# Kernel optimization log

Measured on AMD Instinct MI355X. Metric: run time of the kernel, lower is better.

The kernel has to match this reference:

```python
import jax, jax.numpy as jnp
import numpy as np

VOCAB = 32000   # vocab size
EDIM = 1024     # embedding dim
HDIM = 1024     # encoder hidden dim (fhid dim)
NACTS = 2       # ACTS = {'push': 0, 'pop': 1}
NCLASSES = 3
L = 256         # len_total
B = 128         # bsz
PAD = 0         # padding_idx
PUSH, POP = 0, 1


def setup_inputs() -> dict:
    key = jax.random.key(0)
    ks = jax.random.split(key, 10)

    def mk_seq(kt, kl):
        tok = jax.random.randint(kt, (L, B), 1, VOCAB)          # non-pad tokens
        lens = jax.random.randint(kl, (B,), L // 2, L - 1)      # ragged lengths
        t = jnp.arange(L)[:, None]
        # first lens+1 positions non-pad (so lens = L - n_pad - 1 as in the module)
        return jnp.where(t < lens[None, :] + 1, tok, PAD)

    seq1 = mk_seq(ks[0], ks[1])
    seq2 = mk_seq(ks[2], ks[3])

    def w(k, shp):
        return (jax.random.normal(k, shp, jnp.float32) * 0.02)

    return {
        "seq1": seq1, "seq2": seq2,
        "emb": w(ks[4], (VOCAB, EDIM)),
        "W_top": w(ks[5], (EDIM, HDIM)), "b_top": jnp.zeros((HDIM,), jnp.float32),
        "W_act": w(ks[6], (EDIM, NACTS)), "b_act": jnp.zeros((NACTS,), jnp.float32),
        "W1": w(ks[7], (4 * HDIM, HDIM)), "b1": jnp.zeros((HDIM,), jnp.float32),
        "W2": w(ks[8], (HDIM, NCLASSES)), "b2": jnp.zeros((NCLASSES,), jnp.float32),
    }


def _encode(seq, emb, W_top, b_top, W_act, b_act):
    # stub stack-encoder: time dim 2L-1 (one shift + one reduce step per token)
    seq_ext = jnp.concatenate([seq, seq[:-1]], axis=0)          # [2L-1, B]
    x = emb[seq_ext]                                            # [2L-1, B, E]
    top = jnp.tanh(jnp.einsum('tbe,eh->tbh', x, W_top) + b_top) # [2L-1, B, H]
    act = jax.nn.softmax(jnp.einsum('tbe,ea->tba', x, W_act) + b_act, axis=-1)
    return top, act


def _ragged_stats(act, Ts, bsz):
    # masked equivalents of the per-sample python loops over acts[:T, b, :]
    Tmax = act.shape[0]
    mask = (jnp.arange(Tmax)[:, None] < Ts[None, :]).astype(act.dtype)  # [2L-1, B]
    Tf = Ts.astype(act.dtype)
    push, pop = act[:, :, PUSH], act[:, :, POP]
    sum_push = (push * mask).sum(axis=0) / Tf                   # [B]
    sum_pop = ((pop * mask).sum(axis=0) + 1.0) / Tf             # [B]
    diff = jnp.sqrt((((push - pop) ** 2) * mask).sum(axis=0)) / Tf  # [B]
    dis = jnp.linalg.norm(sum_push - sum_pop) / bsz             # scalar
    return dis, diff.sum() / bsz


def reference(seq1, seq2, emb, W_top, b_top, W_act, b_act, W1, b1, W2, b2):
    bsz = seq1.shape[1]
    top1, act1 = _encode(seq1, emb, W_top, b_top, W_act, b_act)
    top2, act2 = _encode(seq2, emb, W_top, b_top, W_act, b_act)

    lens1 = seq1.shape[0] - (seq1 == PAD).sum(axis=0) - 1
    lens2 = seq2.shape[0] - (seq2 == PAD).sum(axis=0) - 1
    Ts1 = 2 * lens1 - 1
    Ts2 = 2 * lens2 - 1

    barange = jnp.arange(bsz)
    fhid1 = top1[Ts1 - 1, barange]                              # [B, H] ragged gather
    fhid2 = top2[Ts2 - 1, barange]

    u = jnp.concatenate([fhid1, fhid2, jnp.abs(fhid1 - fhid2), fhid1 * fhid2], axis=-1)
    res_clf = jax.nn.relu(u @ W1 + b1) @ W2 + b2                # [B, nclasses]

    dis1, diff1 = _ragged_stats(act1, Ts1, bsz)
    dis2, diff2 = _ragged_stats(act2, Ts2, bsz)
    return (res_clf, dis1, dis2, diff1, diff2)
```

## Files before the change

### kernel.cpp

```cpp
#include <hip/hip_runtime.h>
#include <math.h>

#define LL 256
#define BB 128
#define EDIM 1024
#define HDIM 1024
#define VOCAB 32000

#define NKSF 8
#define NKS  16

#define WS_EACT   0
#define WS_DELTA  32000
#define WS_DIFFB  32256
#define WS_FHID   33024
#define WS_BIG    295168

#define APAD 68

__device__ __forceinline__ void fma4(float4& a, float s, const float4& w) {
  a.x = fmaf(s, w.x, a.x); a.y = fmaf(s, w.y, a.y);
  a.z = fmaf(s, w.z, a.z); a.w = fmaf(s, w.w, a.w);
}

extern "C" __global__ __launch_bounds__(256)
void k_fh_eact(const float* __restrict__ emb, const float* __restrict__ Wtop,
               const float* __restrict__ Wact,
               const int* __restrict__ seq1, const int* __restrict__ seq2,
               float* __restrict__ fpart, float* __restrict__ Eact) {
  __shared__ float ash[128 * APAD];
  __shared__ int stok[128];
  int blk = blockIdx.x, tid = threadIdx.x;
  if (blk >= 256) {
    int lane = tid & 63, wave = tid >> 6;
    int v = (blk - 256) * 4 + wave;
    const float4* row = (const float4*)(emb + (size_t)v * EDIM);
    const float4* w4 = (const float4*)Wact;
    float a0 = 0.f;
#pragma unroll
    for (int it = 0; it < 4; ++it) {
      int i = lane + it * 64;
      float4 x = row[i];
      float4 wa = w4[2 * i];
      float4 wb = w4[2 * i + 1];
      a0 = fmaf(x.x, wa.x - wa.y, a0);
      a0 = fmaf(x.y, wa.z - wa.w, a0);
      a0 = fmaf(x.z, wb.x - wb.y, a0);
      a0 = fmaf(x.w, wb.z - wb.w, a0);
    }
#pragma unroll
    for (int off = 32; off; off >>= 1)
      a0 += __shfl_down(a0, off, 64);
    if (lane == 0) Eact[v] = a0;
    return;
  }
  int ks = blk >> 5, rb = (blk >> 4) & 1, cb = blk & 15;
  int cg = tid & 15, rgr = tid >> 4;
  int c0 = cb * 64 + cg * 4;
  int kbase = ks * 128;
  const int* seq = rb ? seq2 : seq1;
  {
    int c = tid >> 1, h = tid & 1;
    int z = 0;
    int base = h * 128;
    for (int r = 0; r < 128; ++r)
      z += (seq[(base + r) * BB + c] == 0) ? 1 : 0;
    z += __shfl_xor(z, 1, 64);
    if (h == 0) {
      int lens = 255 - z;
      int tt = 2 * lens - 2;
      int idx = (tt < LL) ? tt : tt - LL;
      stok[c] = seq[idx * BB + c];
    }
  }
  float4 acc[8];
#pragma unroll
  for (int r = 0; r < 8; ++r) acc[r] = make_float4(0.f, 0.f, 0.f, 0.f);
#pragma unroll
  for (int ch = 0; ch < 2; ++ch) {
    int kg = kbase + ch * 64;
    __syncthreads();
    for (int idx = tid; idx < 128 * 16; idx += 256) {
      int r = idx >> 4, q = idx & 15;
      *(float4*)&ash[r * APAD + q * 4] =
          ((const float4*)(emb + (size_t)stok[r] * EDIM + kg))[q];
    }
    __syncthreads();
    const float* Wp = Wtop + (size_t)kg * HDIM + c0;
    float4 w[4];
#pragma unroll
    for (int j = 0; j < 4; ++j) w[j] = *(const float4*)(Wp + (size_t)j * HDIM);
#pragma unroll
    for (int kk = 0; kk < 64; kk += 4) {
      float4 wn[4];
      if (kk + 4 < 64) {
#pragma unroll
        for (int j = 0; j < 4; ++j) wn[j] = *(const float4*)(Wp + (size_t)(kk + 4 + j) * HDIM);
      }
#pragma unroll
      for (int r = 0; r < 8; ++r) {
        float4 a = *(const float4*)&ash[(rgr * 8 + r) * APAD + kk];
        fma4(acc[r], a.x, w[0]); fma4(acc[r], a.y, w[1]);
        fma4(acc[r], a.z, w[2]); fma4(acc[r], a.w, w[3]);
      }
#pragma unroll
      for (int j = 0; j < 4; ++j) w[j] = wn[j];
    }
  }
  float* dst = fpart + ((size_t)ks * 256 + rb * 128 + rgr * 8) * HDIM + c0;
#pragma unroll
  for (int r = 0; r < 8; ++r)
    *(float4*)(dst + (size_t)r * HDIM) = acc[r];
}

extern "C" __global__ __launch_bounds__(256)
void k_ftanh_stats(const float* __restrict__ fpart, const float* __restrict__ btop,
                   const int* __restrict__ seq1, const int* __restrict__ seq2,
                   const float* __restrict__ Eact, const float* __restrict__ b_act,
                   float* __restrict__ fhid, float* __restrict__ delta,
                   float* __restrict__ diffb) {
  int blk = blockIdx.x, tid = threadIdx.x;
  if (blk < 256) {
    int g = blk * 256 + tid;
    float4 s = ((const float4*)fpart)[g];
#pragma unroll
    for (int k = 1; k < NKSF; ++k) {
      float4 p = ((const float4*)fpart)[(size_t)k * 65536 + g];
      s.x += p.x; s.y += p.y; s.z += p.z; s.w += p.w;
    }
    float4 b = ((const float4*)btop)[g & 255];
    ((float4*)fhid)[g] = make_float4(tanhf(s.x + b.x), tanhf(s.y + b.y),
                                     tanhf(s.z + b.z), tanhf(s.w + b.w));
    return;
  }
  int sb = blk - 256;
  int s = sb >> 7, b = sb & 127;
  const int* seq = s ? seq2 : seq1;
  __shared__ int col[LL];
  __shared__ int zred[256];
  __shared__ float redf[256];
  int v = seq[tid * BB + b];
  col[tid] = v;
  zred[tid] = (v == 0) ? 1 : 0;
  __syncthreads();
  for (int off = 128; off; off >>= 1) {
    if (tid < off) zred[tid] += zred[tid + off];
    __syncthreads();
  }
  int lens = LL - zred[0] - 1;
  int Ts = 2 * lens - 1;
  float ba = b_act[0] - b_act[1];
  float sp = 0.f, sq = 0.f;
  for (int t = tid; t < Ts; t += 256) {
    int tok = (t < LL) ? col[t] : col[t - LL];
    float d = Eact[tok] + ba;
    float p0 = 1.0f / (1.0f + expf(-d));
    float dd = 2.f * p0 - 1.f;
    sp += dd;
    sq = fmaf(dd, dd, sq);
  }
  redf[tid] = sp; __syncthreads();
  for (int off = 128; off; off >>= 1) { if (tid < off) redf[tid] += redf[tid + off]; __syncthreads(); }
  float tsp = redf[0]; __syncthreads();
  redf[tid] = sq; __syncthreads();
  for (int off = 128; off; off >>= 1) { if (tid < off) redf[tid] += redf[tid + off]; __syncthreads(); }
  if (tid == 0) {
    float Tf = (float)Ts;
    delta[sb] = (tsp - 1.0f) / Tf;
    diffb[sb] = sqrtf(redf[0]) / Tf;
  }
}

extern "C" __global__ __launch_bounds__(256)
void k_part(const float* __restrict__ fhid, const float* __restrict__ W1,
            float* __restrict__ part) {
  __shared__ float ush[64 * APAD];
  int blk = blockIdx.x, tid = threadIdx.x;
  int g = blk >> 1, rh = blk & 1;
  int ksb = g >> 4, cb = g & 15;
  int cg = tid & 15, rgr = tid >> 4;
  int c0 = cb * 64 + cg * 4;
  int m0 = rh * 64;
  int seg = ksb >> 2;
  const float4* f4 = (const float4*)fhid;
  float4 acc[4];
#pragma unroll
  for (int r = 0; r < 4; ++r) acc[r] = make_float4(0.f, 0.f, 0.f, 0.f);
  for (int kch = 0; kch < 4; ++kch) {
    int kg = ksb * 256 + kch * 64;
    int fb4 = (kg & 1023) >> 2;
    __syncthreads();
#pragma unroll
    for (int j = 0; j < 4; ++j) {
      int idx = tid + j * 256;
      int r = idx >> 4, q = idx & 15;
      int row = m0 + r;
      float4 uv;
      if (seg == 0) uv = f4[row * 256 + fb4 + q];
      else if (seg == 1) uv = f4[(128 + row) * 256 + fb4 + q];
      else {
        float4 f1v = f4[row * 256 + fb4 + q];
        float4 f2v = f4[(128 + row) * 256 + fb4 + q];
        if (seg == 2)
          uv = make_float4(fabsf(f1v.x - f2v.x), fabsf(f1v.y - f2v.y),
                           fabsf(f1v.z - f2v.z), fabsf(f1v.w - f2v.w));
        else
          uv = make_float4(f1v.x * f2v.x, f1v.y * f2v.y,
                           f1v.z * f2v.z, f1v.w * f2v.w);
      }
      *(float4*)&ush[r * APAD + q * 4] = uv;
    }
    __syncthreads();
    const float* Wp = W1 + (size_t)kg * HDIM + c0;
    float4 w[4];
#pragma unroll
    for (int j = 0; j < 4; ++j) w[j] = *(const float4*)(Wp + (size_t)j * HDIM);
#pragma unroll
    for (int kk = 0; kk < 64; kk += 4) {
      float4 wn[4];
      if (kk + 4 < 64) {
#pragma unroll
        for (int j = 0; j < 4; ++j)
          wn[j] = *(const float4*)(Wp + (size_t)(kk + 4 + j) * HDIM);
      }
#pragma unroll
      for (int r = 0; r < 4; ++r) {
        float4 a = *(const float4*)&ush[(rgr + 16 * r) * APAD + kk];
        fma4(acc[r], a.x, w[0]); fma4(acc[r], a.y, w[1]);
        fma4(acc[r], a.z, w[2]); fma4(acc[r], a.w, w[3]);
      }
#pragma unroll
      for (int j = 0; j < 4; ++j) w[j] = wn[j];
    }
  }
  float* dst = part + ((size_t)ksb * 128 + m0 + rgr) * HDIM + c0;
#pragma unroll
  for (int r = 0; r < 4; ++r)
    *(float4*)(dst + (size_t)r * 16 * HDIM) = acc[r];
}

extern "C" __global__ __launch_bounds__(256)
void k_clf_final(const float* __restrict__ part, const float* __restrict__ b1,
                 const float* __restrict__ W2, const float* __restrict__ b2,
                 const float* __restrict__ delta, const float* __restrict__ diffb,
                 float* __restrict__ out) {
  int blk = blockIdx.x, tid = threadIdx.x;
  __shared__ float red[768];
  if (blk == 128) {
    for (int s = 0; s < 2; ++s) {
      float v = 0.f, w = 0.f;
      if (tid < BB) { float d = delta[s * BB + tid]; v = d * d; w = diffb[s * BB + tid]; }
      red[tid] = v; __syncthreads();
      for (int off = 128; off; off >>= 1) { if (tid < off) red[tid] += red[tid + off]; __syncthreads(); }
      if (tid == 0) out[384 + s] = sqrtf(red[0]) / (float)BB;
      __syncthreads();
      red[tid] = w; __syncthreads();
      for (int off = 128; off; off >>= 1) { if (tid < off) red[tid] += red[tid + off]; __syncthreads(); }
      if (tid == 0) out[386 + s] = red[0] / (float)BB;
      __syncthreads();
    }
    return;
  }
  int b = blk;
  float4 p = ((const float4*)b1)[tid];
  const float4* p4 = (const float4*)part;
#pragma unroll
  for (int ks = 0; ks < NKS; ++ks) {
    float4 q = p4[((size_t)ks * 128 + b) * 256 + tid];
    p.x += q.x; p.y += q.y; p.z += q.z; p.w += q.w;
  }
  p.x = fmaxf(p.x, 0.f); p.y = fmaxf(p.y, 0.f);
  p.z = fmaxf(p.z, 0.f); p.w = fmaxf(p.w, 0.f);
  int k0 = tid * 4;
  float a0 = 0.f, a1 = 0.f, a2 = 0.f;
  a0 = fmaf(p.x, W2[(k0 + 0) * 3 + 0], a0); a1 = fmaf(p.x, W2[(k0 + 0) * 3 + 1], a1); a2 = fmaf(p.x, W2[(k0 + 0) * 3 + 2], a2);
  a0 = fmaf(p.y, W2[(k0 + 1) * 3 + 0], a0); a1 = fmaf(p.y, W2[(k0 + 1) * 3 + 1], a1); a2 = fmaf(p.y, W2[(k0 + 1) * 3 + 2], a2);
  a0 = fmaf(p.z, W2[(k0 + 2) * 3 + 0], a0); a1 = fmaf(p.z, W2[(k0 + 2) * 3 + 1], a1); a2 = fmaf(p.z, W2[(k0 + 2) * 3 + 2], a2);
  a0 = fmaf(p.w, W2[(k0 + 3) * 3 + 0], a0); a1 = fmaf(p.w, W2[(k0 + 3) * 3 + 1], a1); a2 = fmaf(p.w, W2[(k0 + 3) * 3 + 2], a2);
  red[tid] = a0; red[256 + tid] = a1; red[512 + tid] = a2;
  __syncthreads();
  for (int off = 128; off; off >>= 1) {
    if (tid < off) {
      red[tid] += red[tid + off];
      red[256 + tid] += red[256 + tid + off];
      red[512 + tid] += red[512 + tid + off];
    }
    __syncthreads();
  }
  if (tid == 0) {
    out[b * 3 + 0] = red[0]   + b2[0];
    out[b * 3 + 1] = red[256] + b2[1];
    out[b * 3 + 2] = red[512] + b2[2];
  }
}

extern "C" void kernel_launch(void* const* d_in, const int* in_sizes, int n_in,
                              void* d_out, int out_size, void* d_ws, size_t ws_size,
                              hipStream_t stream) {
  const int*   seq1  = (const int*)  d_in[0];
  const int*   seq2  = (const int*)  d_in[1];
  const float* emb   = (const float*)d_in[2];
  const float* W_top = (const float*)d_in[3];
  const float* b_top = (const float*)d_in[4];
  const float* W_act = (const float*)d_in[5];
  const float* b_act = (const float*)d_in[6];
  const float* W1    = (const float*)d_in[7];
  const float* b1    = (const float*)d_in[8];
  const float* W2    = (const float*)d_in[9];
  const float* b2    = (const float*)d_in[10];
  float* out = (float*)d_out;
  float* ws  = (float*)d_ws;

  float* Eact  = ws + WS_EACT;
  float* delta = ws + WS_DELTA;
  float* diffb = ws + WS_DIFFB;
  float* fhid  = ws + WS_FHID;
  float* bigb  = ws + WS_BIG;

  hipLaunchKernelGGL(k_fh_eact,     dim3(256 + 8000), dim3(256), 0, stream, emb, W_top, W_act, seq1, seq2, bigb, Eact);
  hipLaunchKernelGGL(k_ftanh_stats, dim3(512),        dim3(256), 0, stream, bigb, b_top, seq1, seq2, Eact, b_act, fhid, delta, diffb);
  hipLaunchKernelGGL(k_part,        dim3(512),        dim3(256), 0, stream, fhid, W1, bigb);
  hipLaunchKernelGGL(k_clf_final,   dim3(129),        dim3(256), 0, stream, bigb, b1, W2, b2, delta, diffb, out);
}
```

Baseline: 259.1 us.

## Retile W1 GEMM over all rows and fold ragged stats into it

The W1 partial-product kernel is retiled so each block covers all 128 batch rows over a 128-wide K slice, doubling the split-K count to 32. Each W1 tile is now read by one block instead of two row-halves. The per-sample ragged statistics move out of the tanh-reduction kernel and run as extra blocks of the GEMM launch, so they overlap with GEMM work. The first GEMM's shared-memory row mapping is also interleaved to ease LDS bank conflicts. The cost is twice as many partial sums for the final kernel to reduce, plus higher register use from 8 accumulators per thread.

```diff
diff --git a/kernel.cpp b/kernel.cpp
--- a/kernel.cpp
+++ b/kernel.cpp
@@ -8,7 +8,7 @@
 #define VOCAB 32000
 
 #define NKSF 8
-#define NKS  16
+#define NKS  32
 
 #define WS_EACT   0
 #define WS_DELTA  32000
@@ -99,7 +99,7 @@
       }
 #pragma unroll
       for (int r = 0; r < 8; ++r) {
-        float4 a = *(const float4*)&ash[(rgr * 8 + r) * APAD + kk];
+        float4 a = *(const float4*)&ash[(rgr + 16 * r) * APAD + kk];
         fma4(acc[r], a.x, w[0]); fma4(acc[r], a.y, w[1]);
         fma4(acc[r], a.z, w[2]); fma4(acc[r], a.w, w[3]);
       }
@@ -107,100 +107,99 @@
       for (int j = 0; j < 4; ++j) w[j] = wn[j];
     }
   }
-  float* dst = fpart + ((size_t)ks * 256 + rb * 128 + rgr * 8) * HDIM + c0;
+  float* dst = fpart + ((size_t)ks * 256 + rb * 128 + rgr) * HDIM + c0;
 #pragma unroll
   for (int r = 0; r < 8; ++r)
-    *(float4*)(dst + (size_t)r * HDIM) = acc[r];
+    *(float4*)(dst + (size_t)r * 16 * HDIM) = acc[r];
 }
 
 extern "C" __global__ __launch_bounds__(256)
-void k_ftanh_stats(const float* __restrict__ fpart, const float* __restrict__ btop,
-                   const int* __restrict__ seq1, const int* __restrict__ seq2,
-                   const float* __restrict__ Eact, const float* __restrict__ b_act,
-                   float* __restrict__ fhid, float* __restrict__ delta,
-                   float* __restrict__ diffb) {
+void k_ftanh(const float* __restrict__ fpart, const float* __restrict__ btop,
+             float* __restrict__ fhid) {
   int blk = blockIdx.x, tid = threadIdx.x;
-  if (blk < 256) {
-    int g = blk * 256 + tid;
-    float4 s = ((const float4*)fpart)[g];
-#pragma unroll
-    for (int k = 1; k < NKSF; ++k) {
-      float4 p = ((const float4*)fpart)[(size_t)k * 65536 + g];
-      s.x += p.x; s.y += p.y; s.z += p.z; s.w += p.w;
-    }
-    float4 b = ((const float4*)btop)[g & 255];
-    ((float4*)fhid)[g] = make_float4(tanhf(s.x + b.x), tanhf(s.y + b.y),
-                                     tanhf(s.z + b.z), tanhf(s.w + b.w));
+  int g = blk * 256 + tid;
+  float4 s = ((const float4*)fpart)[g];
+#pragma unroll
+  for (int k = 1; k < NKSF; ++k) {
+    float4 p = ((const float4*)fpart)[(size_t)k * 65536 + g];
+    s.x += p.x; s.y += p.y; s.z += p.z; s.w += p.w;
+  }
+  float4 b = ((const float4*)btop)[g & 255];
+  ((float4*)fhid)[g] = make_float4(tanhf(s.x + b.x), tanhf(s.y + b.y),
+                                   tanhf(s.z + b.z), tanhf(s.w + b.w));
+}
+
+extern "C" __global__ __launch_bounds__(256)
+void k_part_stats(const float* __restrict__ fhid, const float* __restrict__ W1,
+                  const int* __restrict__ seq1, const int* __restrict__ seq2,
+                  const float* __restrict__ Eact, const float* __restrict__ b_act,
+                  float* __restrict__ part, float* __restrict__ delta,
+                  float* __restrict__ diffb) {
+  __shared__ float ash[128 * APAD];
+  __shared__ int col[LL];
+  __shared__ float redf[256];
+  int blk = blockIdx.x, tid = threadIdx.x;
+  if (blk >= 512) {
+    int sb = blk - 512;
+    int s = sb >> 7, b = sb & 127;
+    const int* seq = s ? seq2 : seq1;
+    int* zred = (int*)ash;
+    int v = seq[tid * BB + b];
+    col[tid] = v;
+    zred[tid] = (v == 0) ? 1 : 0;
+    __syncthreads();
+    for (int off = 128; off; off >>= 1) {
+      if (tid < off) zred[tid] += zred[tid + off];
+      __syncthreads();
+    }
+    int lens = LL - zred[0] - 1;
+    int Ts = 2 * lens - 1;
+    float ba = b_act[0] - b_act[1];
+    float sp = 0.f, sq = 0.f;
+    for (int t = tid; t < Ts; t += 256) {
+      int tok = (t < LL) ? col[t] : col[t - LL];
+      float d = Eact[tok] + ba;
+      float p0 = 1.0f / (1.0f + expf(-d));
+      float dd = 2.f * p0 - 1.f;
+      sp += dd;
+      sq = fmaf(dd, dd, sq);
+    }
+    redf[tid] = sp; __syncthreads();
+    for (int off = 128; off; off >>= 1) { if (tid < off) redf[tid] += redf[tid + off]; __syncthreads(); }
+    float tsp = redf[0]; __syncthreads();
+    redf[tid] = sq; __syncthreads();
+    for (int off = 128; off; off >>= 1) { if (tid < off) redf[tid] += redf[tid + off]; __syncthreads(); }
+    if (tid == 0) {
+      float Tf = (float)Ts;
+      delta[sb] = (tsp - 1.0f) / Tf;
+      diffb[sb] = sqrtf(redf[0]) / Tf;
+    }
     return;
   }
-  int sb = blk - 256;
-  int s = sb >> 7, b = sb & 127;
-  const int* seq = s ? seq2 : seq1;
-  __shared__ int col[LL];
-  __shared__ int zred[256];
-  __shared__ float redf[256];
-  int v = seq[tid * BB + b];
-  col[tid] = v;
-  zred[tid] = (v == 0) ? 1 : 0;
-  __syncthreads();
-  for (int off = 128; off; off >>= 1) {
-    if (tid < off) zred[tid] += zred[tid + off];
-    __syncthreads();
-  }
-  int lens = LL - zred[0] - 1;
-  int Ts = 2 * lens - 1;
-  float ba = b_act[0] - b_act[1];
-  float sp = 0.f, sq = 0.f;
-  for (int t = tid; t < Ts; t += 256) {
-    int tok = (t < LL) ? col[t] : col[t - LL];
-    float d = Eact[tok] + ba;
-    float p0 = 1.0f / (1.0f + expf(-d));
-    float dd = 2.f * p0 - 1.f;
-    sp += dd;
-    sq = fmaf(dd, dd, sq);
-  }
-  redf[tid] = sp; __syncthreads();
-  for (int off = 128; off; off >>= 1) { if (tid < off) redf[tid] += redf[tid + off]; __syncthreads(); }
-  float tsp = redf[0]; __syncthreads();
-  redf[tid] = sq; __syncthreads();
-  for (int off = 128; off; off >>= 1) { if (tid < off) redf[tid] += redf[tid + off]; __syncthreads(); }
-  if (tid == 0) {
-    float Tf = (float)Ts;
-    delta[sb] = (tsp - 1.0f) / Tf;
-    diffb[sb] = sqrtf(redf[0]) / Tf;
-  }
-}
-
-extern "C" __global__ __launch_bounds__(256)
-void k_part(const float* __restrict__ fhid, const float* __restrict__ W1,
-            float* __restrict__ part) {
-  __shared__ float ush[64 * APAD];
-  int blk = blockIdx.x, tid = threadIdx.x;
-  int g = blk >> 1, rh = blk & 1;
-  int ksb = g >> 4, cb = g & 15;
+  int ksb = blk >> 4, cb = blk & 15;
   int cg = tid & 15, rgr = tid >> 4;
   int c0 = cb * 64 + cg * 4;
-  int m0 = rh * 64;
-  int seg = ksb >> 2;
+  int kbase = ksb * 128;
+  int seg = ksb >> 3;
   const float4* f4 = (const float4*)fhid;
-  float4 acc[4];
-#pragma unroll
-  for (int r = 0; r < 4; ++r) acc[r] = make_float4(0.f, 0.f, 0.f, 0.f);
-  for (int kch = 0; kch < 4; ++kch) {
-    int kg = ksb * 256 + kch * 64;
+  float4 acc[8];
+#pragma unroll
+  for (int r = 0; r < 8; ++r) acc[r] = make_float4(0.f, 0.f, 0.f, 0.f);
+#pragma unroll
+  for (int kch = 0; kch < 2; ++kch) {
+    int kg = kbase + kch * 64;
     int fb4 = (kg & 1023) >> 2;
     __syncthreads();
 #pragma unroll
-    for (int j = 0; j < 4; ++j) {
+    for (int j = 0; j < 8; ++j) {
       int idx = tid + j * 256;
       int r = idx >> 4, q = idx & 15;
-      int row = m0 + r;
       float4 uv;
-      if (seg == 0) uv = f4[row * 256 + fb4 + q];
-      else if (seg == 1) uv = f4[(128 + row) * 256 + fb4 + q];
+      if (seg == 0) uv = f4[r * 256 + fb4 + q];
+      else if (seg == 1) uv = f4[(128 + r) * 256 + fb4 + q];
       else {
-        float4 f1v = f4[row * 256 + fb4 + q];
-        float4 f2v = f4[(128 + row) * 256 + fb4 + q];
+        float4 f1v = f4[r * 256 + fb4 + q];
+        float4 f2v = f4[(128 + r) * 256 + fb4 + q];
         if (seg == 2)
           uv = make_float4(fabsf(f1v.x - f2v.x), fabsf(f1v.y - f2v.y),
                            fabsf(f1v.z - f2v.z), fabsf(f1v.w - f2v.w));
@@ -208,7 +207,7 @@
           uv = make_float4(f1v.x * f2v.x, f1v.y * f2v.y,
                            f1v.z * f2v.z, f1v.w * f2v.w);
       }
-      *(float4*)&ush[r * APAD + q * 4] = uv;
+      *(float4*)&ash[r * APAD + q * 4] = uv;
     }
     __syncthreads();
     const float* Wp = W1 + (size_t)kg * HDIM + c0;
@@ -224,8 +223,8 @@
           wn[j] = *(const float4*)(Wp + (size_t)(kk + 4 + j) * HDIM);
       }
 #pragma unroll
-      for (int r = 0; r < 4; ++r) {
-        float4 a = *(const float4*)&ush[(rgr + 16 * r) * APAD + kk];
+      for (int r = 0; r < 8; ++r) {
+        float4 a = *(const float4*)&ash[(rgr + 16 * r) * APAD + kk];
         fma4(acc[r], a.x, w[0]); fma4(acc[r], a.y, w[1]);
         fma4(acc[r], a.z, w[2]); fma4(acc[r], a.w, w[3]);
       }
@@ -233,9 +232,9 @@
       for (int j = 0; j < 4; ++j) w[j] = wn[j];
     }
   }
-  float* dst = part + ((size_t)ksb * 128 + m0 + rgr) * HDIM + c0;
-#pragma unroll
-  for (int r = 0; r < 4; ++r)
+  float* dst = part + ((size_t)ksb * 128 + rgr) * HDIM + c0;
+#pragma unroll
+  for (int r = 0; r < 8; ++r)
     *(float4*)(dst + (size_t)r * 16 * HDIM) = acc[r];
 }
 
@@ -317,8 +316,8 @@
   float* fhid  = ws + WS_FHID;
   float* bigb  = ws + WS_BIG;
 
-  hipLaunchKernelGGL(k_fh_eact,     dim3(256 + 8000), dim3(256), 0, stream, emb, W_top, W_act, seq1, seq2, bigb, Eact);
-  hipLaunchKernelGGL(k_ftanh_stats, dim3(512),        dim3(256), 0, stream, bigb, b_top, seq1, seq2, Eact, b_act, fhid, delta, diffb);
-  hipLaunchKernelGGL(k_part,        dim3(512),        dim3(256), 0, stream, fhid, W1, bigb);
-  hipLaunchKernelGGL(k_clf_final,   dim3(129),        dim3(256), 0, stream, bigb, b1, W2, b2, delta, diffb, out);
-}
+  hipLaunchKernelGGL(k_fh_eact,    dim3(256 + 8000), dim3(256), 0, stream, emb, W_top, W_act, seq1, seq2, bigb, Eact);
+  hipLaunchKernelGGL(k_ftanh,      dim3(256),        dim3(256), 0, stream, bigb, b_top, fhid);
+  hipLaunchKernelGGL(k_part_stats, dim3(768),        dim3(256), 0, stream, fhid, W1, seq1, seq2, Eact, b_act, bigb, delta, diffb);
+  hipLaunchKernelGGL(k_clf_final,  dim3(129),        dim3(256), 0, stream, bigb, b1, W2, b2, delta, diffb, out);
+}
```

Result: slower. 266.7 us (+2.9%).

## Spread vocab Eact projection across three kernels and fuse stats into final kernel

Applied to the files above, without the earlier changes.

The per-vocab W_act projection (Eact over all 32000 rows) is split into three chunks. Each chunk rides along as extra blocks in the first three kernels, so the bandwidth-heavy emb scan overlaps with the GEMM-like work instead of sitting mostly in the first kernel. The ragged activation stats move into the final classifier kernel and are reduced with atomics plus a last-block-done counter, which removes the separate delta/diffb workspace and the single-block reduction. The atomic float accumulation makes the reduction order nondeterministic, and it relies on the accumulator being zeroed early in the first kernel.

```diff
diff --git a/kernel.cpp b/kernel.cpp
--- a/kernel.cpp
+++ b/kernel.cpp
@@ -10,9 +10,12 @@
 #define NKSF 8
 #define NKS  16
 
+#define E1 3000
+#define E2 1000
+#define E3 4000
+
 #define WS_EACT   0
-#define WS_DELTA  32000
-#define WS_DIFFB  32256
+#define WS_ACC    32512
 #define WS_FHID   33024
 #define WS_BIG    295168
 
@@ -23,35 +26,44 @@
   a.z = fmaf(s, w.z, a.z); a.w = fmaf(s, w.w, a.w);
 }
 
+__device__ __forceinline__ void eact_row(const float* __restrict__ emb,
+                                         const float* __restrict__ Wact,
+                                         float* __restrict__ Eact,
+                                         int v, int lane) {
+  const float4* row = (const float4*)(emb + (size_t)v * EDIM);
+  const float4* w4 = (const float4*)Wact;
+  float a0 = 0.f;
+#pragma unroll
+  for (int it = 0; it < 4; ++it) {
+    int i = lane + it * 64;
+    float4 x = row[i];
+    float4 wa = w4[2 * i];
+    float4 wb = w4[2 * i + 1];
+    a0 = fmaf(x.x, wa.x - wa.y, a0);
+    a0 = fmaf(x.y, wa.z - wa.w, a0);
+    a0 = fmaf(x.z, wb.x - wb.y, a0);
+    a0 = fmaf(x.w, wb.z - wb.w, a0);
+  }
+#pragma unroll
+  for (int off = 32; off; off >>= 1)
+    a0 += __shfl_down(a0, off, 64);
+  if (lane == 0) Eact[v] = a0;
+}
+
 extern "C" __global__ __launch_bounds__(256)
-void k_fh_eact(const float* __restrict__ emb, const float* __restrict__ Wtop,
-               const float* __restrict__ Wact,
-               const int* __restrict__ seq1, const int* __restrict__ seq2,
-               float* __restrict__ fpart, float* __restrict__ Eact) {
+void k_fh_a(const float* __restrict__ emb, const float* __restrict__ Wtop,
+            const float* __restrict__ Wact,
+            const int* __restrict__ seq1, const int* __restrict__ seq2,
+            float* __restrict__ fpart, float* __restrict__ Eact,
+            float* __restrict__ accbuf) {
   __shared__ float ash[128 * APAD];
   __shared__ int stok[128];
   int blk = blockIdx.x, tid = threadIdx.x;
   if (blk >= 256) {
+    if (blk == 256 && tid < 8) accbuf[tid] = 0.f;
     int lane = tid & 63, wave = tid >> 6;
     int v = (blk - 256) * 4 + wave;
-    const float4* row = (const float4*)(emb + (size_t)v * EDIM);
-    const float4* w4 = (const float4*)Wact;
-    float a0 = 0.f;
-#pragma unroll
-    for (int it = 0; it < 4; ++it) {
-      int i = lane + it * 64;
-      float4 x = row[i];
-      float4 wa = w4[2 * i];
-      float4 wb = w4[2 * i + 1];
-      a0 = fmaf(x.x, wa.x - wa.y, a0);
-      a0 = fmaf(x.y, wa.z - wa.w, a0);
-      a0 = fmaf(x.z, wb.x - wb.y, a0);
-      a0 = fmaf(x.w, wb.z - wb.w, a0);
-    }
-#pragma unroll
-    for (int off = 32; off; off >>= 1)
-      a0 += __shfl_down(a0, off, 64);
-    if (lane == 0) Eact[v] = a0;
+    eact_row(emb, Wact, Eact, v, lane);
     return;
   }
   int ks = blk >> 5, rb = (blk >> 4) & 1, cb = blk & 15;
@@ -114,68 +126,42 @@
 }
 
 extern "C" __global__ __launch_bounds__(256)
-void k_ftanh_stats(const float* __restrict__ fpart, const float* __restrict__ btop,
-                   const int* __restrict__ seq1, const int* __restrict__ seq2,
-                   const float* __restrict__ Eact, const float* __restrict__ b_act,
-                   float* __restrict__ fhid, float* __restrict__ delta,
-                   float* __restrict__ diffb) {
+void k_tanh_b(const float* __restrict__ fpart, const float* __restrict__ btop,
+              float* __restrict__ fhid,
+              const float* __restrict__ emb, const float* __restrict__ Wact,
+              float* __restrict__ Eact) {
   int blk = blockIdx.x, tid = threadIdx.x;
-  if (blk < 256) {
-    int g = blk * 256 + tid;
-    float4 s = ((const float4*)fpart)[g];
-#pragma unroll
-    for (int k = 1; k < NKSF; ++k) {
-      float4 p = ((const float4*)fpart)[(size_t)k * 65536 + g];
-      s.x += p.x; s.y += p.y; s.z += p.z; s.w += p.w;
-    }
-    float4 b = ((const float4*)btop)[g & 255];
-    ((float4*)fhid)[g] = make_float4(tanhf(s.x + b.x), tanhf(s.y + b.y),
-                                     tanhf(s.z + b.z), tanhf(s.w + b.w));
+  if (blk >= 256) {
+    int lane = tid & 63, wave = tid >> 6;
+    int v = 12000 + (blk - 256) * 4 + wave;
+    eact_row(emb, Wact, Eact, v, lane);
     return;
   }
-  int sb = blk - 256;
-  int s = sb >> 7, b = sb & 127;
-  const int* seq = s ? seq2 : seq1;
-  __shared__ int col[LL];
-  __shared__ int zred[256];
-  __shared__ float redf[256];
-  int v = seq[tid * BB + b];
-  col[tid] = v;
-  zred[tid] = (v == 0) ? 1 : 0;
-  __syncthreads();
-  for (int off = 128; off; off >>= 1) {
-    if (tid < off) zred[tid] += zred[tid + off];
-    __syncthreads();
-  }
-  int lens = LL - zred[0] - 1;
-  int Ts = 2 * lens - 1;
-  float ba = b_act[0] - b_act[1];
-  float sp = 0.f, sq = 0.f;
-  for (int t = tid; t < Ts; t += 256) {
-    int tok = (t < LL) ? col[t] : col[t - LL];
-    float d = Eact[tok] + ba;
-    float p0 = 1.0f / (1.0f + expf(-d));
-    float dd = 2.f * p0 - 1.f;
-    sp += dd;
-    sq = fmaf(dd, dd, sq);
-  }
-  redf[tid] = sp; __syncthreads();
-  for (int off = 128; off; off >>= 1) { if (tid < off) redf[tid] += redf[tid + off]; __syncthreads(); }
-  float tsp = redf[0]; __syncthreads();
-  redf[tid] = sq; __syncthreads();
-  for (int off = 128; off; off >>= 1) { if (tid < off) redf[tid] += redf[tid + off]; __syncthreads(); }
-  if (tid == 0) {
-    float Tf = (float)Ts;
-    delta[sb] = (tsp - 1.0f) / Tf;
-    diffb[sb] = sqrtf(redf[0]) / Tf;
-  }
+  int g = blk * 256 + tid;
+  float4 s = ((const float4*)fpart)[g];
+#pragma unroll
+  for (int k = 1; k < NKSF; ++k) {
+    float4 p = ((const float4*)fpart)[(size_t)k * 65536 + g];
+    s.x += p.x; s.y += p.y; s.z += p.z; s.w += p.w;
+  }
+  float4 b = ((const float4*)btop)[g & 255];
+  ((float4*)fhid)[g] = make_float4(tanhf(s.x + b.x), tanhf(s.y + b.y),
+                                   tanhf(s.z + b.z), tanhf(s.w + b.w));
 }
 
 extern "C" __global__ __launch_bounds__(256)
-void k_part(const float* __restrict__ fhid, const float* __restrict__ W1,
-            float* __restrict__ part) {
+void k_part_c(const float* __restrict__ fhid, const float* __restrict__ W1,
+              float* __restrict__ part,
+              const float* __restrict__ emb, const float* __restrict__ Wact,
+              float* __restrict__ Eact) {
   __shared__ float ush[64 * APAD];
   int blk = blockIdx.x, tid = threadIdx.x;
+  if (blk >= 512) {
+    int lane = tid & 63, wave = tid >> 6;
+    int v = 16000 + (blk - 512) * 4 + wave;
+    eact_row(emb, Wact, Eact, v, lane);
+    return;
+  }
   int g = blk >> 1, rh = blk & 1;
   int ksb = g >> 4, cb = g & 15;
   int cg = tid & 15, rgr = tid >> 4;
@@ -240,24 +226,64 @@
 }
 
 extern "C" __global__ __launch_bounds__(256)
-void k_clf_final(const float* __restrict__ part, const float* __restrict__ b1,
+void k_clf_stats(const float* __restrict__ part, const float* __restrict__ b1,
                  const float* __restrict__ W2, const float* __restrict__ b2,
-                 const float* __restrict__ delta, const float* __restrict__ diffb,
-                 float* __restrict__ out) {
+                 const int* __restrict__ seq1, const int* __restrict__ seq2,
+                 const float* __restrict__ Eact, const float* __restrict__ b_act,
+                 float* __restrict__ accbuf, float* __restrict__ out) {
   int blk = blockIdx.x, tid = threadIdx.x;
   __shared__ float red[768];
-  if (blk == 128) {
-    for (int s = 0; s < 2; ++s) {
-      float v = 0.f, w = 0.f;
-      if (tid < BB) { float d = delta[s * BB + tid]; v = d * d; w = diffb[s * BB + tid]; }
-      red[tid] = v; __syncthreads();
-      for (int off = 128; off; off >>= 1) { if (tid < off) red[tid] += red[tid + off]; __syncthreads(); }
-      if (tid == 0) out[384 + s] = sqrtf(red[0]) / (float)BB;
+  if (blk >= 128) {
+    int sb = blk - 128;
+    int s = sb >> 7, b = sb & 127;
+    const int* seq = s ? seq2 : seq1;
+    int* col = (int*)red;
+    int* zred = (int*)(red + 256);
+    float* redf = red + 512;
+    int v = seq[tid * BB + b];
+    col[tid] = v;
+    zred[tid] = (v == 0) ? 1 : 0;
+    __syncthreads();
+    for (int off = 128; off; off >>= 1) {
+      if (tid < off) zred[tid] += zred[tid + off];
       __syncthreads();
-      red[tid] = w; __syncthreads();
-      for (int off = 128; off; off >>= 1) { if (tid < off) red[tid] += red[tid + off]; __syncthreads(); }
-      if (tid == 0) out[386 + s] = red[0] / (float)BB;
-      __syncthreads();
+    }
+    int lens = LL - zred[0] - 1;
+    int Ts = 2 * lens - 1;
+    float ba = b_act[0] - b_act[1];
+    float sp = 0.f, sq = 0.f;
+    for (int t = tid; t < Ts; t += 256) {
+      int tok = (t < LL) ? col[t] : col[t - LL];
+      float d = Eact[tok] + ba;
+      float p0 = 1.0f / (1.0f + expf(-d));
+      float dd = 2.f * p0 - 1.f;
+      sp += dd;
+      sq = fmaf(dd, dd, sq);
+    }
+    redf[tid] = sp; __syncthreads();
+    for (int off = 128; off; off >>= 1) { if (tid < off) redf[tid] += redf[tid + off]; __syncthreads(); }
+    float tsp = redf[0]; __syncthreads();
+    redf[tid] = sq; __syncthreads();
+    for (int off = 128; off; off >>= 1) { if (tid < off) redf[tid] += redf[tid + off]; __syncthreads(); }
+    if (tid == 0) {
+      float Tf = (float)Ts;
+      float delta = (tsp - 1.0f) / Tf;
+      float dfb = sqrtf(redf[0]) / Tf;
+      atomicAdd(&accbuf[s], delta * delta);
+      atomicAdd(&accbuf[2 + s], dfb);
+      __threadfence();
+      int old = atomicAdd((int*)(accbuf + 4), 1);
+      if (old == 255) {
+        __threadfence();
+        float d0 = atomicAdd(&accbuf[0], 0.f);
+        float d1 = atomicAdd(&accbuf[1], 0.f);
+        float f0 = atomicAdd(&accbuf[2], 0.f);
+        float f1 = atomicAdd(&accbuf[3], 0.f);
+        out[384] = sqrtf(d0) / (float)BB;
+        out[385] = sqrtf(d1) / (float)BB;
+        out[386] = f0 / (float)BB;
+        out[387] = f1 / (float)BB;
+      }
     }
     return;
   }
@@ -312,13 +338,12 @@
   float* ws  = (float*)d_ws;
 
   float* Eact  = ws + WS_EACT;
-  float* delta = ws + WS_DELTA;
-  float* diffb = ws + WS_DIFFB;
+  float* accb  = ws + WS_ACC;
   float* fhid  = ws + WS_FHID;
   float* bigb  = ws + WS_BIG;
 
-  hipLaunchKernelGGL(k_fh_eact,     dim3(256 + 8000), dim3(256), 0, stream, emb, W_top, W_act, seq1, seq2, bigb, Eact);
-  hipLaunchKernelGGL(k_ftanh_stats, dim3(512),        dim3(256), 0, stream, bigb, b_top, seq1, seq2, Eact, b_act, fhid, delta, diffb);
-  hipLaunchKernelGGL(k_part,        dim3(512),        dim3(256), 0, stream, fhid, W1, bigb);
-  hipLaunchKernelGGL(k_clf_final,   dim3(129),        dim3(256), 0, stream, bigb, b1, W2, b2, delta, diffb, out);
-}
+  hipLaunchKernelGGL(k_fh_a,     dim3(256 + E1), dim3(256), 0, stream, emb, W_top, W_act, seq1, seq2, bigb, Eact, accb);
+  hipLaunchKernelGGL(k_tanh_b,   dim3(256 + E2), dim3(256), 0, stream, bigb, b_top, fhid, emb, W_act, Eact);
+  hipLaunchKernelGGL(k_part_c,   dim3(512 + E3), dim3(256), 0, stream, fhid, W1, bigb, emb, W_act, Eact);
+  hipLaunchKernelGGL(k_clf_stats,dim3(384),      dim3(256), 0, stream, bigb, b1, W2, b2, seq1, seq2, Eact, b_act, accb, out);
+}
```

After: 274.7 us. 6.0% more time.
